# Kernel tuning notes

Measured on AMD Instinct MI355X. Metric: run time of the kernel, lower is better.

Reference implementation:

```python
import jax, jax.numpy as jnp
import numpy as np

B, N, MODES, WIDTH = 4, 8192, 12, 32
TWO = 2 * MODES  # 24
M_TOT = TWO * (TWO - 1)  # 552


def setup_inputs() -> dict:
    key = jax.random.key(0)
    ks = jax.random.split(key, 12)
    scale = 1.0 / (WIDTH * WIDTH)
    x = jax.random.uniform(ks[0], (B, N, 2), jnp.float32)
    fc0_w = jax.random.normal(ks[1], (2, WIDTH), jnp.float32) * 0.1
    fc0_b = jax.random.normal(ks[2], (WIDTH,), jnp.float32) * 0.05
    # 4 layers x {weights1, weights2}, stored as real/imag pairs (torch.rand cfloat ~ U[0,1)+1j*U[0,1))
    spec_w = jax.random.uniform(ks[3], (4, 2, WIDTH, WIDTH, MODES, MODES, 2), jnp.float32) * scale
    conv_w = jax.random.normal(ks[4], (4, WIDTH, WIDTH), jnp.float32) * 0.1  # Conv1d k=1 -> [O,I]
    conv_b = jax.random.normal(ks[5], (4, WIDTH), jnp.float32) * 0.05
    fc1_w = jax.random.normal(ks[6], (WIDTH, 128), jnp.float32) * 0.1
    fc1_b = jax.random.normal(ks[7], (128,), jnp.float32) * 0.05
    fc2_w = jax.random.normal(ks[8], (128, 1), jnp.float32) * 0.1
    fc2_b = jax.random.normal(ks[9], (1,), jnp.float32) * 0.05
    return {"x": x, "fc0_w": fc0_w, "fc0_b": fc0_b, "spec_w": spec_w,
            "conv_w": conv_w, "conv_b": conv_b, "fc1_w": fc1_w, "fc1_b": fc1_b,
            "fc2_w": fc2_w, "fc2_b": fc2_b}


def _vft_matrices(xp, yp):
    # xp, yp: [B, N], already min-shifted and scaled to [0, 6.28]
    kx = jnp.concatenate([jnp.arange(MODES), jnp.arange(-MODES, 0)]).astype(jnp.float32)       # [24]
    ky = jnp.concatenate([jnp.arange(MODES), jnp.arange(-(MODES - 1), 0)]).astype(jnp.float32)  # [23]
    Xm = kx[None, :, None] * xp[:, None, :]  # [B,24,N]
    Ym = ky[None, :, None] * yp[:, None, :]  # [B,23,N]
    # torch: X repeat(1,23,1) tiles blocks; Y repeat(1,1,24).reshape interleaves -> row j*24+i = X[i]+Y[j]
    phase = jnp.tile(Xm, (1, TWO - 1, 1)) + jnp.repeat(Ym, TWO, axis=1)  # [B,552,N]
    V_fwd = jnp.exp(-1j * phase)                    # [B,552,N] complex64
    V_inv = jnp.conj(V_fwd).transpose(0, 2, 1)      # [B,N,552]
    return V_fwd, V_inv


def _spectral_conv(h, V_fwd, V_inv, w1, w2):
    # h: [B,C,N] real; w1,w2: [C,C,M,M] complex
    b, c, n = h.shape
    # forward Vandermonde transform: bmm(V_fwd, h^T) then permute -> [B,C,552]
    x_ft = jnp.einsum('bmn,bnc->bcm', V_fwd, h.astype(jnp.complex64).transpose(0, 2, 1))
    x_ft = x_ft.reshape(b, c, TWO, TWO - 1)
    top = jnp.einsum('bixy,ioxy->boxy', x_ft[:, :, :MODES, :MODES], w1)
    bot = jnp.einsum('bixy,ioxy->boxy', x_ft[:, :, -MODES:, :MODES], w2)
    out_ft = jnp.zeros((b, WIDTH, TWO, MODES), jnp.complex64)
    out_ft = out_ft.at[:, :, :MODES, :MODES].set(top)
    out_ft = out_ft.at[:, :, -MODES:, :MODES].set(bot)
    x_ft = out_ft.reshape(b, WIDTH, 2 * MODES * MODES)  # [B,C,288]
    # conjugate-symmetric completion (flip over last two dims, as in source)
    x_ft2 = jnp.conj(jnp.flip(x_ft[..., TWO:], axis=(-2, -1)))  # [B,C,264]
    x_ft = jnp.concatenate([x_ft, x_ft2], axis=-1)  # [B,C,552]
    out = jnp.einsum('bnm,bmc->bcn', V_inv, x_ft.transpose(0, 2, 1))  # [B,C,N]
    return (out / n * 2).real


def reference(x, fc0_w, fc0_b, spec_w, conv_w, conv_b, fc1_w, fc1_b, fc2_w, fc2_b):
    gelu = lambda t: jax.nn.gelu(t, approximate=False)
    # VFT mutates x in-place by subtracting global mins (view semantics in torch)
    xp = x[:, :, 0] - jnp.min(x[:, :, 0])
    yp = x[:, :, 1] - jnp.min(x[:, :, 1])
    x_in = jnp.stack([xp, yp], axis=-1)  # what fc0 actually sees
    V_fwd, V_inv = _vft_matrices(xp * 6.28 / jnp.max(xp), yp * 6.28 / jnp.max(yp))
    h = (x_in @ fc0_w + fc0_b).transpose(0, 2, 1)  # [B,C,N]
    for l in range(4):
        w1 = spec_w[l, 0, ..., 0] + 1j * spec_w[l, 0, ..., 1]
        w2 = spec_w[l, 1, ..., 0] + 1j * spec_w[l, 1, ..., 1]
        x1 = _spectral_conv(h, V_fwd, V_inv, w1, w2)
        x2 = jnp.einsum('bin,oi->bon', h, conv_w[l]) + conv_b[l][None, :, None]
        h = x1 + x2
        if l < 3:
            h = gelu(h)
    h = h.transpose(0, 2, 1)  # [B,N,C]
    h = gelu(h @ fc1_w + fc1_b)
    return h @ fc2_w + fc2_b  # [B,N,1]
```

## Files before the change

### kernel.cpp

```cpp
#include <hip/hip_runtime.h>
#include <cmath>

#define NB 4
#define NN 8192
#define CH 32

typedef short short8 __attribute__((ext_vector_type(8)));
typedef float floatx4 __attribute__((ext_vector_type(4)));
typedef unsigned short ushort_t;

__device__ __forceinline__ unsigned short f2b(float f){
  unsigned u = __float_as_uint(f);
  u = u + 0x7FFFu + ((u >> 16) & 1u);
  return (unsigned short)(u >> 16);
}
__device__ __forceinline__ float b2f(unsigned short h){
  return __uint_as_float(((unsigned)h) << 16);
}
__device__ __forceinline__ float gelu_f(float v){
  return 0.5f * v * (1.0f + erff(v * 0.70710678118654752440f));
}
__device__ __forceinline__ int repk(int t){
  int j = t / 24, i = t - j * 24;
  if(j == 0)  return (i <= 12) ? i : -1;
  if(j <= 11) return 13 + (j - 1) * 24 + i;
  return (i == 12) ? 277 + (j - 12) : -1;
}
__device__ __forceinline__ int partner(int t){
  int j = t / 24, i = t - j * 24;
  return ((23 - j) % 23) * 24 + ((24 - i) % 24);
}
__device__ __forceinline__ int repT(int k){
  if(k < 13) return k;
  if(k < 277){ int m = k - 13; return (m / 24 + 1) * 24 + (m % 24); }
  return (k - 277 + 12) * 24 + 12;
}

__global__ __launch_bounds__(256) void k_pre(const float* __restrict__ spec,
    float2* __restrict__ wt, const float* __restrict__ x, float4* __restrict__ pmm,
    const float* __restrict__ fc1w, ushort_t* __restrict__ WB,
    const float* __restrict__ convw, ushort_t* __restrict__ WA)
{
  const int tid = threadIdx.x;
  if(blockIdx.x < 128){
    int g = blockIdx.x * 256 + tid;
    float a = x[(size_t)g * 2], b = x[(size_t)g * 2 + 1];
    float mn0 = a, mx0 = a, mn1 = b, mx1 = b;
    for(int off = 32; off > 0; off >>= 1){
      mn0 = fminf(mn0, __shfl_down(mn0, off));
      mx0 = fmaxf(mx0, __shfl_down(mx0, off));
      mn1 = fminf(mn1, __shfl_down(mn1, off));
      mx1 = fmaxf(mx1, __shfl_down(mx1, off));
    }
    __shared__ float4 wp[4];
    if((tid & 63) == 0) wp[tid >> 6] = make_float4(mn0, mn1, mx0, mx1);
    __syncthreads();
    if(tid == 0){
      float4 r = wp[0];
      for(int i2 = 1; i2 < 4; ++i2){
        float4 v = wp[i2];
        r.x = fminf(r.x, v.x); r.y = fminf(r.y, v.y);
        r.z = fmaxf(r.z, v.z); r.w = fmaxf(r.w, v.w);
      }
      pmm[blockIdx.x] = r;
    }
  } else if(blockIdx.x < 4736){
    int g = (blockIdx.x - 128) * 256 + tid;
    int o  = g & 31;
    int i  = (g >> 5) & 31;
    int rest = g >> 10;
    int pq = rest % 144;
    int ls = rest / 144;
    wt[g] = ((const float2*)spec)[(((size_t)(ls * 32 + i) * 32 + o) * 144 + pq)];
  } else {
    for(int s = tid; s < 512; s += 256){
      int jt = s >> 6, l = s & 63;
      int c = l & 15, qq = l >> 4;
      #pragma unroll
      for(int e = 0; e < 8; ++e){
        float wv = fc1w[(qq * 8 + e) * 128 + jt * 16 + c];
        ushort_t hi = f2b(wv);
        WB[(jt * 64 + l) * 8 + e] = hi;
        WB[4096 + (jt * 64 + l) * 8 + e] = f2b(wv - b2f(hi));
      }
    }
    for(int s = tid; s < 8192; s += 256){
      int l2   = s >> 11;
      int rem  = s & 2047;
      int limb = rem >> 10;
      int rem2 = rem & 1023;
      int half = rem2 >> 9;
      int le   = rem2 & 511;
      int lane = le >> 3, e = le & 7;
      int c = half * 16 + (lane & 15);
      int i = (lane >> 4) * 8 + e;
      float wv = convw[((size_t)l2 * 32 + c) * 32 + i] * 4096.0f;
      ushort_t hi = f2b(wv);
      WA[s] = limb ? f2b(wv - b2f(hi)) : hi;
    }
  }
}

__global__ __launch_bounds__(256) void k_vbuild(const float* __restrict__ x,
    const float4* __restrict__ pmm, const float* __restrict__ fw,
    const float* __restrict__ fb, ushort_t* __restrict__ AF, ushort_t* __restrict__ VTF,
    ushort_t* __restrict__ hbB, ushort_t* __restrict__ hbChi, ushort_t* __restrict__ hbClo)
{
  __shared__ ushort_t lds1[32 * 584];
  __shared__ float4 mmv;
  const int tid = threadIdx.x;
  if(tid < 64){
    float4 a = pmm[tid], c = pmm[tid + 64];
    float mn0 = fminf(a.x, c.x), mn1 = fminf(a.y, c.y);
    float mx0 = fmaxf(a.z, c.z), mx1 = fmaxf(a.w, c.w);
    for(int off = 32; off > 0; off >>= 1){
      mn0 = fminf(mn0, __shfl_down(mn0, off));
      mn1 = fminf(mn1, __shfl_down(mn1, off));
      mx0 = fmaxf(mx0, __shfl_down(mx0, off));
      mx1 = fmaxf(mx1, __shfl_down(mx1, off));
    }
    if(tid == 0) mmv = make_float4(mn0, mn1, mx0, mx1);
  }
  __syncthreads();
  const int nl = tid & 31, part = tid >> 5;
  const int b = blockIdx.x >> 8;
  const int nblk = blockIdx.x & 255;
  const int n = nblk * 32 + nl;
  float mn0 = mmv.x, mn1 = mmv.y, mx0 = mmv.z, mx1 = mmv.w;
  float x0 = x[(size_t)(b * NN + n) * 2]     - mn0;
  float x1 = x[(size_t)(b * NN + n) * 2 + 1] - mn1;
  float sp = x0 * (6.28f / (mx0 - mn0));
  float sq = x1 * (6.28f / (mx1 - mn1));
  float cx, sx, cy, sy;
  sincosf(sp, &sx, &cx);
  sincosf(sq, &sy, &cy);
  int j0 = part * 3;
  int j1 = (j0 + 3 < 23) ? j0 + 3 : 23;
  float ky0 = (j0 < 12) ? (float)j0 : (float)(j0 - 23);
  float cb, sb;
  sincosf(ky0 * sq, &sb, &cb);
  for(int j = j0; j < j1; ++j){
    float ca = 1.0f, sa = 0.0f;
    #pragma unroll
    for(int i = 0; i < 24; ++i){
      float vr = ca * cb - sa * sb;
      float vi = -(sa * cb + ca * sb);
      int t = j * 24 + i;
      int k = repk(t);
      if(k >= 0){
        lds1[nl * 584 + k]       = f2b(vr);
        lds1[nl * 584 + 288 + k] = f2b(vi);
      }
      float cn = ca * cx - sa * sx;
      float sn = sa * cx + ca * sx;
      if(i == 11) sn = -sn;
      ca = cn; sa = sn;
    }
    float cbn = cb * cy - sb * sy;
    float sbn = sb * cy + cb * sy;
    cb = cbn; sb = sbn;
  }
  __syncthreads();
  #pragma unroll
  for(int r = 0; r < 9; ++r){
    int c = tid + 256 * r;
    int t16 = c / 1152;
    int c2 = c - t16 * 1152;
    int kk = c2 >> 6;
    int rem = c2 & 63;
    int q = rem >> 4, n15 = rem & 15;
    short8 v = *(const short8*)(lds1 + (t16 * 16 + n15) * 584 + kk * 32 + q * 8);
    *(short8*)(VTF + ((size_t)((b * 512 + nblk * 2 + t16) * 18 + kk)) * 512
               + (q * 16 + n15) * 8) = v;
  }
  #pragma unroll
  for(int r = 0; r < 9; ++r){
    int c = tid + 256 * r;
    int st = c >> 6;
    int rem = c & 63;
    int q = rem >> 4, srow = rem & 15;
    int sg = st * 16 + srow;
    int s = (sg < 288) ? sg : sg - 288;
    int sinh_ = (sg >= 288);
    int p2 = s / 12, qq = s - p2 * 12;
    int t = p2 * 23 + qq;
    int k = repk(t);
    unsigned short flip = 0;
    if(k < 0){ k = repk(partner(t)); if(sinh_) flip = 0x8000; }
    int col = sinh_ ? 288 + k : k;
    ushort_t tmp[8];
    #pragma unroll
    for(int e = 0; e < 8; ++e)
      tmp[e] = lds1[(q * 8 + e) * 584 + col] ^ flip;
    *(short8*)(AF + ((size_t)((b * 36 + st) * 256 + nblk)) * 512
               + (q * 16 + srow) * 8) = *(short8*)tmp;
  }
  #pragma unroll
  for(int rr = 0; rr < 4; ++rr){
    int c2 = part + rr * 8;
    float v = fb[c2] + x0 * fw[c2] + x1 * fw[32 + c2];
    ushort_t hi = f2b(v), lo = f2b(v - b2f(hi));
    int half = c2 >> 4, cl = c2 & 15;
    hbB[(((size_t)(b * 2 + half) * 256 + nblk) * 512) + ((nl >> 3) * 16 + cl) * 8 + (nl & 7)] = hi;
    size_t ca = ((size_t)(b * 512 + nblk * 2 + (nl >> 4))) * 512
              + ((c2 >> 3) * 16 + (nl & 15)) * 8 + (c2 & 7);
    hbChi[ca] = hi; hbClo[ca] = lo;
  }
}

__global__ __launch_bounds__(256) void k_fwd(const ushort_t* __restrict__ AF,
    const ushort_t* __restrict__ hbB, float* __restrict__ xp)
{
  const int stp = blockIdx.x;
  const int ks = blockIdx.y;
  const int b  = blockIdx.z;
  const int w = threadIdx.x >> 6;
  const int lane = threadIdx.x & 63;
  const int row = lane & 15;
  const int q = lane >> 4;
  const int st0 = stp * 2;
  const size_t abase0 = ((size_t)(b * 36 + st0) * 256) * 512 + (q * 16 + row) * 8;
  const size_t abase1 = abase0 + (size_t)256 * 512;
  const size_t hB0 = ((size_t)(b * 2 + 0) * 256) * 512 + (size_t)lane * 8;
  const size_t hB1 = ((size_t)(b * 2 + 1) * 256) * 512 + (size_t)lane * 8;
  floatx4 aA0 = {0.f,0.f,0.f,0.f}, aA1 = {0.f,0.f,0.f,0.f};
  floatx4 aB0 = {0.f,0.f,0.f,0.f}, aB1 = {0.f,0.f,0.f,0.f};
  #pragma unroll
  for(int kk = 0; kk < 4; ++kk){
    int g = ks * 16 + w * 4 + kk;
    short8 A0 = *(const short8*)(AF + abase0 + (size_t)g * 512);
    short8 A1 = *(const short8*)(AF + abase1 + (size_t)g * 512);
    short8 B0 = *(const short8*)(hbB + hB0 + (size_t)g * 512);
    short8 B1 = *(const short8*)(hbB + hB1 + (size_t)g * 512);
    aA0 = __builtin_amdgcn_mfma_f32_16x16x32_bf16(A0, B0, aA0, 0, 0, 0);
    aA1 = __builtin_amdgcn_mfma_f32_16x16x32_bf16(A0, B1, aA1, 0, 0, 0);
    aB0 = __builtin_amdgcn_mfma_f32_16x16x32_bf16(A1, B0, aB0, 0, 0, 0);
    aB1 = __builtin_amdgcn_mfma_f32_16x16x32_bf16(A1, B1, aB1, 0, 0, 0);
  }
  __shared__ float red[4 * 512];
  const int e = threadIdx.x;
  const int eo = e & 31;
  #pragma unroll
  for(int r = 0; r < 4; ++r){
    int rrow = q * 4 + r;
    red[w * 512 + rrow * 32 + row]      = aA0[r];
    red[w * 512 + rrow * 32 + 16 + row] = aA1[r];
  }
  __syncthreads();
  {
    float v0 = red[e] + red[512 + e] + red[1024 + e] + red[1536 + e];
    float v1 = red[e + 256] + red[512 + e + 256] + red[1024 + e + 256] + red[1536 + e + 256];
    size_t r0 = (size_t)(b * 576 + st0 * 16 + (e >> 5));
    xp[(r0 * 16 + ks) * 32 + eo]       = v0;
    xp[((r0 + 8) * 16 + ks) * 32 + eo] = v1;
  }
  __syncthreads();
  #pragma unroll
  for(int r = 0; r < 4; ++r){
    int rrow = q * 4 + r;
    red[w * 512 + rrow * 32 + row]      = aB0[r];
    red[w * 512 + rrow * 32 + 16 + row] = aB1[r];
  }
  __syncthreads();
  {
    float v0 = red[e] + red[512 + e] + red[1024 + e] + red[1536 + e];
    float v1 = red[e + 256] + red[512 + e + 256] + red[1024 + e + 256] + red[1536 + e + 256];
    size_t r0 = (size_t)(b * 576 + (st0 + 1) * 16 + (e >> 5));
    xp[(r0 * 16 + ks) * 32 + eo]       = v0;
    xp[((r0 + 8) * 16 + ks) * 32 + eo] = v1;
  }
}

__global__ __launch_bounds__(256) void k_mixg(const float* __restrict__ xp,
    const float2* __restrict__ wt, ushort_t* __restrict__ ghif, ushort_t* __restrict__ glof,
    int layer)
{
  const int wv = threadIdx.x >> 6;
  const int lane = threadIdx.x & 63;
  const int k = blockIdx.x;
  const int b = blockIdx.y;
  const int t = repT(k);
  const int j = t / 24, i = t - j * 24;
  const int u = partner(t);
  const bool unpaired = (i == 12) || (u == t);
  const int idxT = (t < 288) ? t : 575 - t;  const bool cfT = (t >= 288);
  const int idxU = (u < 288) ? u : 575 - u;  const bool cfU = (u >= 288);
  __shared__ float Xs[2][64];
  __shared__ float FrP[2][2][32], FiP[2][2][32];
  {
    const int m = wv & 1, hf = wv >> 1;
    int idx = m ? idxU : idxT;
    int rrow = hf ? 288 + idx : idx;
    const float* sb = xp + (size_t)(b * 576 + rrow) * 512;
    float4 a = *(const float4*)(sb + lane * 4);
    float4 c = *(const float4*)(sb + 256 + lane * 4);
    a.x += c.x; a.y += c.y; a.z += c.z; a.w += c.w;
    #pragma unroll
    for(int mk = 8; mk <= 32; mk <<= 1){
      a.x += __shfl_xor(a.x, mk);
      a.y += __shfl_xor(a.y, mk);
      a.z += __shfl_xor(a.z, mk);
      a.w += __shfl_xor(a.w, mk);
    }
    if(lane < 8){
      int o0 = hf * 32 + lane * 4;
      Xs[m][o0 + 0] = a.x;
      Xs[m][o0 + 1] = a.y;
      Xs[m][o0 + 2] = a.z;
      Xs[m][o0 + 3] = a.w;
    }
  }
  __syncthreads();
  {
    const int m = wv & 1, ih = wv >> 1;
    int idx = m ? idxU : idxT;
    int p2 = idx / 12, qq = idx - p2 * 12;
    int sel = (p2 < 12) ? 0 : 1;
    int pq = (p2 % 12) * 12 + qq;
    const float2* wb = wt + ((size_t)((layer * 2 + sel) * 144 + pq)) * 1024;
    if(lane < 32){
      const int o = lane;
      float fr = 0.f, fi = 0.f;
      #pragma unroll
      for(int ii = 0; ii < 16; ++ii){
        int i2 = ih * 16 + ii;
        float xr = Xs[m][i2], xi = Xs[m][32 + i2];
        float2 wvv = wb[i2 * 32 + o];
        fr += xr * wvv.x - xi * wvv.y;
        fi += xr * wvv.y + xi * wvv.x;
      }
      FrP[m][ih][o] = fr; FiP[m][ih][o] = fi;
    }
  }
  __syncthreads();
  if(wv == 0 && lane < 32){
    const int c = lane;
    const int srcT = cfT ? 31 - c : c;
    const int srcU = cfU ? 31 - c : c;
    float fax = FrP[0][0][srcT] + FrP[0][1][srcT];
    float fay = FiP[0][0][srcT] + FiP[0][1][srcT];
    float fbx = FrP[1][0][srcU] + FrP[1][1][srcU];
    float fby = FiP[1][0][srcU] + FiP[1][1][srcU];
    float gr = fax;
    float gi = cfT ? -fay : fay;
    if(!unpaired){
      gr += fbx;
      gi -= (cfU ? -fby : fby);
    }
    unsigned short hr = f2b(gr); float lr = gr - b2f(hr);
    unsigned short hi2 = f2b(gi); float li = gi - b2f(hi2);
    int hhc = c >> 4, cl = c & 15;
    int kk1 = k >> 5, q1 = (k >> 3) & 3, e1 = k & 7;
    size_t fb2 = (size_t)(b * 2 + hhc) * 18;
    size_t off = (size_t)(q1 * 16 + cl) * 8 + e1;
    ghif[(fb2 + kk1) * 512 + off]     = hr;
    ghif[(fb2 + 9 + kk1) * 512 + off] = hi2;
    glof[(fb2 + kk1) * 512 + off]     = f2b(lr);
    glof[(fb2 + 9 + kk1) * 512 + off] = f2b(li);
  }
}

template<int LAST>
__global__ __launch_bounds__(256, 6) void k_inv(const ushort_t* __restrict__ VTF,
    const ushort_t* __restrict__ ghif, const ushort_t* __restrict__ glof,
    const float* __restrict__ cbias, int layer,
    const ushort_t* __restrict__ hbCi_hi, const ushort_t* __restrict__ hbCi_lo,
    ushort_t* __restrict__ hbBo, ushort_t* __restrict__ hbCo_hi,
    ushort_t* __restrict__ hbCo_lo,
    const float* __restrict__ b1, const float* __restrict__ w2,
    const float* __restrict__ b2, float* __restrict__ out,
    const ushort_t* __restrict__ WBg, const ushort_t* __restrict__ WA)
{
  const int tid = threadIdx.x;
  const int b = blockIdx.y;
  const int bx = blockIdx.x;
  const int lane = tid & 63;
  const int w = tid >> 6;
  const int tl = w >> 1;
  const int hh = w & 1;
  const int row = lane & 15, q = lane >> 4;
  const int t16 = bx * 2 + tl;
  const ushort_t* vb = VTF + ((size_t)(b * 512 + t16) * 18) * 512 + lane * 8;
  const ushort_t* gh = ghif + ((size_t)(b * 2 + hh) * 18) * 512 + lane * 8;
  const ushort_t* gl = glof + ((size_t)(b * 2 + hh) * 18) * 512 + lane * 8;
  floatx4 ah = {0.f,0.f,0.f,0.f}, al = {0.f,0.f,0.f,0.f};
  #pragma unroll
  for(int kk = 0; kk < 18; ++kk){
    short8 Bv = *(const short8*)(vb + (size_t)kk * 512);
    short8 Ah = *(const short8*)(gh + (size_t)kk * 512);
    short8 Al = *(const short8*)(gl + (size_t)kk * 512);
    ah = __builtin_amdgcn_mfma_f32_16x16x32_bf16(Ah, Bv, ah, 0, 0, 0);
    al = __builtin_amdgcn_mfma_f32_16x16x32_bf16(Al, Bv, al, 0, 0, 0);
  }
  {
    short8 Whi = *(const short8*)(WA + ((size_t)((layer * 2 + 0) * 2 + hh)) * 512 + lane * 8);
    short8 Wlo = *(const short8*)(WA + ((size_t)((layer * 2 + 1) * 2 + hh)) * 512 + lane * 8);
    short8 Bhi = *(const short8*)(hbCi_hi + ((size_t)(b * 512 + t16)) * 512 + lane * 8);
    short8 Blo = *(const short8*)(hbCi_lo + ((size_t)(b * 512 + t16)) * 512 + lane * 8);
    ah = __builtin_amdgcn_mfma_f32_16x16x32_bf16(Whi, Bhi, ah, 0, 0, 0);
    al = __builtin_amdgcn_mfma_f32_16x16x32_bf16(Wlo, Bhi, al, 0, 0, 0);
    ah = __builtin_amdgcn_mfma_f32_16x16x32_bf16(Whi, Blo, ah, 0, 0, 0);
  }
  floatx4 accF = ah + al;
  const float sc = 2.0f / 8192.0f;
  float cb[4];
  #pragma unroll
  for(int r = 0; r < 4; ++r) cb[r] = cbias[layer * 32 + hh * 16 + q * 4 + r];
  if constexpr(!LAST){
    const int n = bx * 32 + tl * 16 + row;
    const int g2 = n >> 5, qb = (n >> 3) & 3, e2 = n & 7;
    #pragma unroll
    for(int r = 0; r < 4; ++r){
      int c = hh * 16 + q * 4 + r;
      float v = gelu_f(accF[r] * sc + cb[r]);
      ushort_t hi = f2b(v), lo = f2b(v - b2f(hi));
      hbBo[(((size_t)(b * 2 + hh) * 256 + g2) * 512) + (qb * 16 + (q * 4 + r)) * 8 + e2] = hi;
      size_t ca = ((size_t)(b * 512 + t16)) * 512 + ((c >> 3) * 16 + row) * 8 + (c & 7);
      hbCo_hi[ca] = hi; hbCo_lo[ca] = lo;
    }
  } else {
    __shared__ ushort_t hHi[32][36];
    __shared__ ushort_t hLo[32][36];
    __shared__ float part[2][32];
    {
      ushort_t H[4], L[4];
      #pragma unroll
      for(int r = 0; r < 4; ++r){
        float v = accF[r] * sc + cb[r];
        H[r] = f2b(v); L[r] = f2b(v - b2f(H[r]));
      }
      uint2 uu;
      uu.x = (unsigned)H[0] | ((unsigned)H[1] << 16);
      uu.y = (unsigned)H[2] | ((unsigned)H[3] << 16);
      *(uint2*)&hHi[tl * 16 + row][hh * 16 + q * 4] = uu;
      uu.x = (unsigned)L[0] | ((unsigned)L[1] << 16);
      uu.y = (unsigned)L[2] | ((unsigned)L[3] << 16);
      *(uint2*)&hLo[tl * 16 + row][hh * 16 + q * 4] = uu;
    }
    __syncthreads();
    const int cl = row;
    short8 Ahi = *(const short8*)&hHi[tl * 16 + cl][q * 8];
    short8 Alo = *(const short8*)&hLo[tl * 16 + cl][q * 8];
    float S0 = 0.f, S1 = 0.f, S2 = 0.f, S3 = 0.f;
    #pragma unroll
    for(int jt2 = 0; jt2 < 4; ++jt2){
      int jt = hh * 4 + jt2;
      short8 Bhi = *(const short8*)(WBg + (jt * 64 + lane) * 8);
      short8 Blo = *(const short8*)(WBg + 4096 + (jt * 64 + lane) * 8);
      floatx4 acc = {0.f, 0.f, 0.f, 0.f};
      acc = __builtin_amdgcn_mfma_f32_16x16x32_bf16(Ahi, Bhi, acc, 0, 0, 0);
      acc = __builtin_amdgcn_mfma_f32_16x16x32_bf16(Alo, Bhi, acc, 0, 0, 0);
      acc = __builtin_amdgcn_mfma_f32_16x16x32_bf16(Ahi, Blo, acc, 0, 0, 0);
      float bv = b1[jt * 16 + cl], wv = w2[jt * 16 + cl];
      S0 = fmaf(gelu_f(acc[0] + bv), wv, S0);
      S1 = fmaf(gelu_f(acc[1] + bv), wv, S1);
      S2 = fmaf(gelu_f(acc[2] + bv), wv, S2);
      S3 = fmaf(gelu_f(acc[3] + bv), wv, S3);
    }
    #pragma unroll
    for(int off = 8; off; off >>= 1){
      S0 += __shfl_xor(S0, off, 16);
      S1 += __shfl_xor(S1, off, 16);
      S2 += __shfl_xor(S2, off, 16);
      S3 += __shfl_xor(S3, off, 16);
    }
    if(cl == 0){
      int pb = tl * 16 + q * 4;
      part[hh][pb + 0] = S0;
      part[hh][pb + 1] = S1;
      part[hh][pb + 2] = S2;
      part[hh][pb + 3] = S3;
    }
    __syncthreads();
    if(tid < 32)
      out[(size_t)b * NN + bx * 32 + tid] = part[0][tid] + part[1][tid] + b2[0];
  }
}

extern "C" void kernel_launch(void* const* d_in, const int* in_sizes, int n_in,
                              void* d_out, int out_size, void* d_ws, size_t ws_size,
                              hipStream_t stream)
{
  const float* x      = (const float*)d_in[0];
  const float* fc0_w  = (const float*)d_in[1];
  const float* fc0_b  = (const float*)d_in[2];
  const float* spec_w = (const float*)d_in[3];
  const float* conv_w = (const float*)d_in[4];
  const float* conv_b = (const float*)d_in[5];
  const float* fc1_w  = (const float*)d_in[6];
  const float* fc1_b  = (const float*)d_in[7];
  const float* fc2_w  = (const float*)d_in[8];
  const float* fc2_b  = (const float*)d_in[9];
  float* out = (float*)d_out;

  char* w = (char*)d_ws;
  const size_t OFF_PMM  = 0;
  const size_t OFF_WT   = 4096;
  const size_t OFF_AF   = OFF_WT  + 9437184;
  const size_t OFF_VTF  = OFF_AF  + 37748736;
  const size_t OFF_HB0  = OFF_VTF + 37748736;
  const size_t OFF_HB1  = OFF_HB0 + 2097152;
  const size_t OFF_HC0  = OFF_HB1 + 2097152;
  const size_t OFF_HC1  = OFF_HC0 + 2097152;
  const size_t OFF_HL0  = OFF_HC1 + 2097152;
  const size_t OFF_HL1  = OFF_HL0 + 2097152;
  const size_t OFF_XP   = OFF_HL1 + 2097152;
  const size_t OFF_GHF  = OFF_XP  + 4718592;
  const size_t OFF_GLO  = OFF_GHF + 147456;
  const size_t OFF_WB   = OFF_GLO + 147456;
  const size_t OFF_WA   = OFF_WB  + 16384;

  float4* pmm    = (float4*)(w + OFF_PMM);
  float2* wt     = (float2*)(w + OFF_WT);
  ushort_t* AF   = (ushort_t*)(w + OFF_AF);
  ushort_t* VTF  = (ushort_t*)(w + OFF_VTF);
  ushort_t* hbB[2]  = { (ushort_t*)(w + OFF_HB0), (ushort_t*)(w + OFF_HB1) };
  ushort_t* hbChi[2] = { (ushort_t*)(w + OFF_HC0), (ushort_t*)(w + OFF_HC1) };
  ushort_t* hbClo[2] = { (ushort_t*)(w + OFF_HL0), (ushort_t*)(w + OFF_HL1) };
  float* xp      = (float*)(w + OFF_XP);
  ushort_t* ghif = (ushort_t*)(w + OFF_GHF);
  ushort_t* glof = (ushort_t*)(w + OFF_GLO);
  ushort_t* WB   = (ushort_t*)(w + OFF_WB);
  ushort_t* WA   = (ushort_t*)(w + OFF_WA);

  hipLaunchKernelGGL(k_pre, dim3(4737), dim3(256), 0, stream, spec_w, wt, x, pmm,
                     fc1_w, WB, conv_w, WA);
  hipLaunchKernelGGL(k_vbuild, dim3(1024), dim3(256), 0, stream, x, pmm,
                     fc0_w, fc0_b, AF, VTF, hbB[0], hbChi[0], hbClo[0]);

  for(int l = 0; l < 4; ++l){
    int in = l & 1, outb = 1 - in;
    hipLaunchKernelGGL(k_fwd, dim3(18, 16, NB), dim3(256), 0, stream, AF, hbB[in], xp);
    hipLaunchKernelGGL(k_mixg, dim3(288, NB), dim3(256), 0, stream, xp, wt, ghif, glof, l);
    if(l < 3)
      hipLaunchKernelGGL(k_inv<0>, dim3(256, NB), dim3(256), 0, stream, VTF, ghif, glof,
                         conv_b, l, hbChi[in], hbClo[in],
                         hbB[outb], hbChi[outb], hbClo[outb],
                         fc1_b, fc2_w, fc2_b, out, WB, WA);
    else
      hipLaunchKernelGGL(k_inv<1>, dim3(256, NB), dim3(256), 0, stream, VTF, ghif, glof,
                         conv_b, l, hbChi[in], hbClo[in],
                         hbB[outb], hbChi[outb], hbClo[outb],
                         fc1_b, fc2_w, fc2_b, out, WB, WA);
  }
  (void)in_sizes; (void)n_in; (void)out_size; (void)ws_size;
}
```

Measured before the change: 224.5 us.

## Fuse forward transform and spectral mixing into one kernel per layer

```diff
diff --git a/kernel.cpp b/kernel.cpp
--- a/kernel.cpp
+++ b/kernel.cpp
@@ -208,139 +208,96 @@
   }
 }
 
-__global__ __launch_bounds__(256) void k_fwd(const ushort_t* __restrict__ AF,
-    const ushort_t* __restrict__ hbB, float* __restrict__ xp)
+__global__ __launch_bounds__(512, 2) void k_fm(const ushort_t* __restrict__ AF,
+    const ushort_t* __restrict__ hbB, const float2* __restrict__ wt,
+    ushort_t* __restrict__ ghif, ushort_t* __restrict__ glof, int layer)
 {
-  const int stp = blockIdx.x;
-  const int ks = blockIdx.y;
-  const int b  = blockIdx.z;
-  const int w = threadIdx.x >> 6;
-  const int lane = threadIdx.x & 63;
-  const int row = lane & 15;
-  const int q = lane >> 4;
-  const int st0 = stp * 2;
-  const size_t abase0 = ((size_t)(b * 36 + st0) * 256) * 512 + (q * 16 + row) * 8;
-  const size_t abase1 = abase0 + (size_t)256 * 512;
-  const size_t hB0 = ((size_t)(b * 2 + 0) * 256) * 512 + (size_t)lane * 8;
-  const size_t hB1 = ((size_t)(b * 2 + 1) * 256) * 512 + (size_t)lane * 8;
-  floatx4 aA0 = {0.f,0.f,0.f,0.f}, aA1 = {0.f,0.f,0.f,0.f};
-  floatx4 aB0 = {0.f,0.f,0.f,0.f}, aB1 = {0.f,0.f,0.f,0.f};
-  #pragma unroll
-  for(int kk = 0; kk < 4; ++kk){
-    int g = ks * 16 + w * 4 + kk;
-    short8 A0 = *(const short8*)(AF + abase0 + (size_t)g * 512);
-    short8 A1 = *(const short8*)(AF + abase1 + (size_t)g * 512);
-    short8 B0 = *(const short8*)(hbB + hB0 + (size_t)g * 512);
-    short8 B1 = *(const short8*)(hbB + hB1 + (size_t)g * 512);
-    aA0 = __builtin_amdgcn_mfma_f32_16x16x32_bf16(A0, B0, aA0, 0, 0, 0);
-    aA1 = __builtin_amdgcn_mfma_f32_16x16x32_bf16(A0, B1, aA1, 0, 0, 0);
-    aB0 = __builtin_amdgcn_mfma_f32_16x16x32_bf16(A1, B0, aB0, 0, 0, 0);
-    aB1 = __builtin_amdgcn_mfma_f32_16x16x32_bf16(A1, B1, aB1, 0, 0, 0);
-  }
-  __shared__ float red[4 * 512];
-  const int e = threadIdx.x;
-  const int eo = e & 31;
-  #pragma unroll
-  for(int r = 0; r < 4; ++r){
-    int rrow = q * 4 + r;
-    red[w * 512 + rrow * 32 + row]      = aA0[r];
-    red[w * 512 + rrow * 32 + 16 + row] = aA1[r];
+  const int rq = blockIdx.x;
+  const int b  = blockIdx.y;
+  const int tid = threadIdx.x;
+  const int wv = tid >> 6, lane = tid & 63;
+  const int cl = lane & 15, q = lane >> 4;
+  __shared__ float red[8][16][32];
+  __shared__ float X[16][33];
+  __shared__ float Fr[4][2][32], Fi[4][2][32];
+  {
+    int r4 = cl >> 2, slot = cl & 3;
+    int k0 = rq * 4 + r4;
+    int t0 = repT(k0);
+    int u0 = partner(t0);
+    int idxT0 = (t0 < 288) ? t0 : 575 - t0;
+    int idxU0 = (u0 < 288) ? u0 : 575 - u0;
+    int sg = (slot == 0) ? idxT0 : (slot == 1) ? 288 + idxT0
+           : (slot == 2) ? idxU0 : 288 + idxU0;
+    int st = sg >> 4, srow = sg & 15;
+    const size_t abase = ((size_t)(b * 36 + st) * 256) * 512 + (q * 16 + srow) * 8;
+    const size_t hB0 = ((size_t)(b * 2 + 0) * 256) * 512 + (size_t)lane * 8;
+    const size_t hB1 = ((size_t)(b * 2 + 1) * 256) * 512 + (size_t)lane * 8;
+    floatx4 a0 = {0.f,0.f,0.f,0.f}, a1 = {0.f,0.f,0.f,0.f};
+    #pragma unroll 4
+    for(int gi = 0; gi < 32; ++gi){
+      int g = wv * 32 + gi;
+      short8 Av = *(const short8*)(AF + abase + (size_t)g * 512);
+      short8 B0 = *(const short8*)(hbB + hB0 + (size_t)g * 512);
+      short8 B1 = *(const short8*)(hbB + hB1 + (size_t)g * 512);
+      a0 = __builtin_amdgcn_mfma_f32_16x16x32_bf16(Av, B0, a0, 0, 0, 0);
+      a1 = __builtin_amdgcn_mfma_f32_16x16x32_bf16(Av, B1, a1, 0, 0, 0);
+    }
+    #pragma unroll
+    for(int r = 0; r < 4; ++r){
+      red[wv][q * 4 + r][cl]      = a0[r];
+      red[wv][q * 4 + r][16 + cl] = a1[r];
+    }
   }
   __syncthreads();
   {
-    float v0 = red[e] + red[512 + e] + red[1024 + e] + red[1536 + e];
-    float v1 = red[e + 256] + red[512 + e + 256] + red[1024 + e + 256] + red[1536 + e + 256];
-    size_t r0 = (size_t)(b * 576 + st0 * 16 + (e >> 5));
-    xp[(r0 * 16 + ks) * 32 + eo]       = v0;
-    xp[((r0 + 8) * 16 + ks) * 32 + eo] = v1;
-  }
-  __syncthreads();
-  #pragma unroll
-  for(int r = 0; r < 4; ++r){
-    int rrow = q * 4 + r;
-    red[w * 512 + rrow * 32 + row]      = aB0[r];
-    red[w * 512 + rrow * 32 + 16 + row] = aB1[r];
+    int tr = tid >> 5, o = tid & 31;
+    float s = red[0][tr][o];
+    #pragma unroll
+    for(int w = 1; w < 8; ++w) s += red[w][tr][o];
+    X[tr][o] = s;
   }
   __syncthreads();
   {
-    float v0 = red[e] + red[512 + e] + red[1024 + e] + red[1536 + e];
-    float v1 = red[e + 256] + red[512 + e + 256] + red[1024 + e + 256] + red[1536 + e + 256];
-    size_t r0 = (size_t)(b * 576 + (st0 + 1) * 16 + (e >> 5));
-    xp[(r0 * 16 + ks) * 32 + eo]       = v0;
-    xp[((r0 + 8) * 16 + ks) * 32 + eo] = v1;
-  }
-}
-
-__global__ __launch_bounds__(256) void k_mixg(const float* __restrict__ xp,
-    const float2* __restrict__ wt, ushort_t* __restrict__ ghif, ushort_t* __restrict__ glof,
-    int layer)
-{
-  const int wv = threadIdx.x >> 6;
-  const int lane = threadIdx.x & 63;
-  const int k = blockIdx.x;
-  const int b = blockIdx.y;
-  const int t = repT(k);
-  const int j = t / 24, i = t - j * 24;
-  const int u = partner(t);
-  const bool unpaired = (i == 12) || (u == t);
-  const int idxT = (t < 288) ? t : 575 - t;  const bool cfT = (t >= 288);
-  const int idxU = (u < 288) ? u : 575 - u;  const bool cfU = (u >= 288);
-  __shared__ float Xs[2][64];
-  __shared__ float FrP[2][2][32], FiP[2][2][32];
-  {
-    const int m = wv & 1, hf = wv >> 1;
-    int idx = m ? idxU : idxT;
-    int rrow = hf ? 288 + idx : idx;
-    const float* sb = xp + (size_t)(b * 576 + rrow) * 512;
-    float4 a = *(const float4*)(sb + lane * 4);
-    float4 c = *(const float4*)(sb + 256 + lane * 4);
-    a.x += c.x; a.y += c.y; a.z += c.z; a.w += c.w;
-    #pragma unroll
-    for(int mk = 8; mk <= 32; mk <<= 1){
-      a.x += __shfl_xor(a.x, mk);
-      a.y += __shfl_xor(a.y, mk);
-      a.z += __shfl_xor(a.z, mk);
-      a.w += __shfl_xor(a.w, mk);
-    }
-    if(lane < 8){
-      int o0 = hf * 32 + lane * 4;
-      Xs[m][o0 + 0] = a.x;
-      Xs[m][o0 + 1] = a.y;
-      Xs[m][o0 + 2] = a.z;
-      Xs[m][o0 + 3] = a.w;
-    }
-  }
-  __syncthreads();
-  {
-    const int m = wv & 1, ih = wv >> 1;
-    int idx = m ? idxU : idxT;
+    int r4b = wv >> 1, m = wv & 1;
+    int kb = rq * 4 + r4b;
+    int tb = repT(kb);
+    int ub = partner(tb);
+    int idx = m ? ((ub < 288) ? ub : 575 - ub) : ((tb < 288) ? tb : 575 - tb);
     int p2 = idx / 12, qq = idx - p2 * 12;
     int sel = (p2 < 12) ? 0 : 1;
     int pq = (p2 % 12) * 12 + qq;
     const float2* wb = wt + ((size_t)((layer * 2 + sel) * 144 + pq)) * 1024;
     if(lane < 32){
       const int o = lane;
+      const int rc = r4b * 4 + 2 * m, rs = rc + 1;
       float fr = 0.f, fi = 0.f;
       #pragma unroll
-      for(int ii = 0; ii < 16; ++ii){
-        int i2 = ih * 16 + ii;
-        float xr = Xs[m][i2], xi = Xs[m][32 + i2];
-        float2 wvv = wb[i2 * 32 + o];
+      for(int ii = 0; ii < 32; ++ii){
+        float xr = X[rc][ii], xi = X[rs][ii];
+        float2 wvv = wb[ii * 32 + o];
         fr += xr * wvv.x - xi * wvv.y;
         fi += xr * wvv.y + xi * wvv.x;
       }
-      FrP[m][ih][o] = fr; FiP[m][ih][o] = fi;
+      Fr[r4b][m][o] = fr; Fi[r4b][m][o] = fi;
     }
   }
   __syncthreads();
-  if(wv == 0 && lane < 32){
+  if(wv < 4 && lane < 32){
+    const int k = rq * 4 + wv;
+    const int t = repT(k);
+    const int i = t - (t / 24) * 24;
+    const int u = partner(t);
+    const bool unpaired = (i == 12) || (u == t);
+    const bool cfT = (t >= 288);
+    const bool cfU = (u >= 288);
     const int c = lane;
     const int srcT = cfT ? 31 - c : c;
     const int srcU = cfU ? 31 - c : c;
-    float fax = FrP[0][0][srcT] + FrP[0][1][srcT];
-    float fay = FiP[0][0][srcT] + FiP[0][1][srcT];
-    float fbx = FrP[1][0][srcU] + FrP[1][1][srcU];
-    float fby = FiP[1][0][srcU] + FiP[1][1][srcU];
+    float fax = Fr[wv][0][srcT];
+    float fay = Fi[wv][0][srcT];
+    float fbx = Fr[wv][1][srcU];
+    float fby = Fi[wv][1][srcU];
     float gr = fax;
     float gi = cfT ? -fay : fay;
     if(!unpaired){
@@ -349,10 +306,10 @@
     }
     unsigned short hr = f2b(gr); float lr = gr - b2f(hr);
     unsigned short hi2 = f2b(gi); float li = gi - b2f(hi2);
-    int hhc = c >> 4, cl = c & 15;
+    int hhc = c >> 4, clc = c & 15;
     int kk1 = k >> 5, q1 = (k >> 3) & 3, e1 = k & 7;
     size_t fb2 = (size_t)(b * 2 + hhc) * 18;
-    size_t off = (size_t)(q1 * 16 + cl) * 8 + e1;
+    size_t off = (size_t)(q1 * 16 + clc) * 8 + e1;
     ghif[(fb2 + kk1) * 512 + off]     = hr;
     ghif[(fb2 + 9 + kk1) * 512 + off] = hi2;
     glof[(fb2 + kk1) * 512 + off]     = f2b(lr);
@@ -504,8 +461,7 @@
   const size_t OFF_HC1  = OFF_HC0 + 2097152;
   const size_t OFF_HL0  = OFF_HC1 + 2097152;
   const size_t OFF_HL1  = OFF_HL0 + 2097152;
-  const size_t OFF_XP   = OFF_HL1 + 2097152;
-  const size_t OFF_GHF  = OFF_XP  + 4718592;
+  const size_t OFF_GHF  = OFF_HL1 + 2097152;
   const size_t OFF_GLO  = OFF_GHF + 147456;
   const size_t OFF_WB   = OFF_GLO + 147456;
   const size_t OFF_WA   = OFF_WB  + 16384;
@@ -517,7 +473,6 @@
   ushort_t* hbB[2]  = { (ushort_t*)(w + OFF_HB0), (ushort_t*)(w + OFF_HB1) };
   ushort_t* hbChi[2] = { (ushort_t*)(w + OFF_HC0), (ushort_t*)(w + OFF_HC1) };
   ushort_t* hbClo[2] = { (ushort_t*)(w + OFF_HL0), (ushort_t*)(w + OFF_HL1) };
-  float* xp      = (float*)(w + OFF_XP);
   ushort_t* ghif = (ushort_t*)(w + OFF_GHF);
   ushort_t* glof = (ushort_t*)(w + OFF_GLO);
   ushort_t* WB   = (ushort_t*)(w + OFF_WB);
@@ -530,8 +485,8 @@
 
   for(int l = 0; l < 4; ++l){
     int in = l & 1, outb = 1 - in;
-    hipLaunchKernelGGL(k_fwd, dim3(18, 16, NB), dim3(256), 0, stream, AF, hbB[in], xp);
-    hipLaunchKernelGGL(k_mixg, dim3(288, NB), dim3(256), 0, stream, xp, wt, ghif, glof, l);
+    hipLaunchKernelGGL(k_fm, dim3(72, NB), dim3(512), 0, stream, AF, hbB[in], wt,
+                       ghif, glof, l);
     if(l < 3)
       hipLaunchKernelGGL(k_inv<0>, dim3(256, NB), dim3(256), 0, stream, VTF, ghif, glof,
                          conv_b, l, hbChi[in], hbClo[in],
```

New measurement: 307.7 us. 1.37x slower.
